# Kernel optimization log

Hardware: AMD Instinct MI355X
Metric: run time of the kernel (lower is better)

## Reference

```python
import jax, jax.numpy as jnp
import numpy as np

B, S, H = 8, 1024, 1024
NH, HD = 16, 64
LN_EPS = 1e-12


def setup_inputs() -> dict:
    key = jax.random.key(0)
    ks = jax.random.split(key, 8)
    sd = 0.02
    return {
        "hidden_states": jax.random.normal(ks[0], (B, S, H), jnp.float32),
        "attention_mask": jnp.zeros((B, 1, 1, S), jnp.float32),
        "Wq": jax.random.normal(ks[1], (H, H), jnp.float32) * sd,
        "bq": jnp.zeros((H,), jnp.float32),
        "Wk": jax.random.normal(ks[2], (H, H), jnp.float32) * sd,
        "bk": jnp.zeros((H,), jnp.float32),
        "Wv": jax.random.normal(ks[3], (H, H), jnp.float32) * sd,
        "bv": jnp.zeros((H,), jnp.float32),
        "Wo": jax.random.normal(ks[4], (H, H), jnp.float32) * sd,
        "bo": jnp.zeros((H,), jnp.float32),
        "ln_gamma": jnp.ones((H,), jnp.float32),
        "ln_beta": jnp.zeros((H,), jnp.float32),
    }


def _heads(x):
    # [B,S,H] -> [B,NH,S,HD]
    return x.reshape(B, S, NH, HD).transpose(0, 2, 1, 3)


def reference(hidden_states, attention_mask, Wq, bq, Wk, bk, Wv, bv, Wo, bo, ln_gamma, ln_beta):
    # QKV projections (torch Linear: x @ W.T + b)
    q = _heads(hidden_states @ Wq.T + bq)
    k = _heads(hidden_states @ Wk.T + bk)
    v = _heads(hidden_states @ Wv.T + bv)
    # scaled dot-product attention with additive mask
    scores = jnp.einsum("bhqd,bhkd->bhqk", q, k) / np.sqrt(HD).astype(np.float32)
    scores = scores + attention_mask  # broadcast [B,1,1,S]
    probs = jax.nn.softmax(scores, axis=-1)
    ctx = jnp.einsum("bhqk,bhkd->bhqd", probs, v)
    ctx = ctx.transpose(0, 2, 1, 3).reshape(B, S, H)
    # output projection + residual + LayerNorm
    out = ctx @ Wo.T + bo
    x = out + hidden_states
    mu = jnp.mean(x, axis=-1, keepdims=True)
    var = jnp.var(x, axis=-1, keepdims=True)
    return (x - mu) * jax.lax.rsqrt(var + LN_EPS) * ln_gamma + ln_beta
```

## Files before the change

### kernel.cpp

```cpp
#include <hip/hip_runtime.h>
#include <stdint.h>

typedef __attribute__((ext_vector_type(8))) __bf16 bf16x8;
typedef __attribute__((ext_vector_type(8))) unsigned short ushortx8;
typedef __attribute__((ext_vector_type(4))) unsigned short ushortx4;
typedef __attribute__((ext_vector_type(4))) short short4v;
typedef __attribute__((ext_vector_type(4))) float floatx4;

#define LOG2E 1.4426950408889634f
#define QSCALE 0.18033688011112043f

#define ASYNC16(g, l) __builtin_amdgcn_global_load_lds( \
    (__attribute__((address_space(1))) void*)(g),       \
    (__attribute__((address_space(3))) void*)(l), 16, 0, 0)

__device__ __forceinline__ unsigned short f2bf(float f) {
    unsigned int u = __float_as_uint(f);
    u += 0x7fffu + ((u >> 16) & 1u);
    return (unsigned short)(u >> 16);
}
__device__ __forceinline__ float bf2f(unsigned short u) {
    return __uint_as_float((unsigned)u << 16);
}

__device__ __forceinline__ floatx4 mfma32(bf16x8 a, bf16x8 b, floatx4 c) {
    return __builtin_amdgcn_mfma_f32_16x16x32_bf16(a, b, c, 0, 0, 0);
}
__device__ __forceinline__ floatx4 mfma16(short4v a, short4v b, floatx4 c) {
    return __builtin_amdgcn_mfma_f32_16x16x16bf16_1k(a, b, c, 0, 0, 0);
}

__global__ __launch_bounds__(256) void cvt_all(
    const float* __restrict__ hidden,
    const float* __restrict__ Wq, const float* __restrict__ Wk,
    const float* __restrict__ Wv, const float* __restrict__ Wo,
    unsigned short* __restrict__ hid_bf,
    unsigned short* __restrict__ oqkv, unsigned short* __restrict__ oo)
{
    const float* src;
    unsigned short* dst;
    int i;
    if (blockIdx.x < 4096) {
        src = hidden; dst = hid_bf;
        i = blockIdx.x * 256 + threadIdx.x;
    } else {
        int blk = (blockIdx.x - 4096) >> 9;
        src = (blk == 0) ? Wq : (blk == 1) ? Wk : (blk == 2) ? Wv : Wo;
        dst = (blk == 3) ? oo : oqkv + (size_t)blk * 1048576;
        i = ((blockIdx.x - 4096) & 511) * 256 + threadIdx.x;
    }
    const float4* p = (const float4*)src + (size_t)i * 2;
    float4 a = p[0], b = p[1];
    ushortx8 o;
    o[0] = f2bf(a.x); o[1] = f2bf(a.y); o[2] = f2bf(a.z); o[3] = f2bf(a.w);
    o[4] = f2bf(b.x); o[5] = f2bf(b.y); o[6] = f2bf(b.z); o[7] = f2bf(b.w);
    *((ushortx8*)dst + i) = o;
}

template<bool SWAP>
__device__ __forceinline__ void kloop_dbuf(
    const unsigned short* __restrict__ Ag,
    const unsigned short* __restrict__ Wg,
    unsigned short As[2][8192], unsigned short Bs[2][8192],
    int wm, int wn, int l16, int quad, int t,
    floatx4 acc[4][4])
{
    const int t8 = t * 8;
#define SAx(bf_, i_, kt_) ASYNC16(Ag + (size_t)(i_) * 32 * 1024 + (kt_) * 64, &As[bf_][(i_) * 2048 + t8])
#define SBx(bf_, i_, kt_) ASYNC16(Wg + (size_t)(i_) * 32 * 1024 + (kt_) * 64, &Bs[bf_][(i_) * 2048 + t8])
#pragma unroll
    for (int i = 0; i < 4; i++) { SAx(0, i, 0); SBx(0, i, 0); }
    __syncthreads();

#pragma unroll 1
    for (int kt = 0; kt < 16; ++kt) {
        const int cur = kt & 1, nb = cur ^ 1;
        if (kt < 15) {
#pragma unroll
            for (int i = 0; i < 4; i++) { SAx(nb, i, kt + 1); SBx(nb, i, kt + 1); }
        }
#pragma unroll
        for (int s = 0; s < 2; s++) {
            int pb = ((s * 4 + quad) ^ (l16 & 7)) * 8;
            bf16x8 af[4], bfr[4];
#pragma unroll
            for (int mt = 0; mt < 4; mt++)
                af[mt] = *(const bf16x8*)(&As[cur][(wm + mt * 16 + l16) * 64 + pb]);
#pragma unroll
            for (int nt = 0; nt < 4; nt++)
                bfr[nt] = *(const bf16x8*)(&Bs[cur][(wn + nt * 16 + l16) * 64 + pb]);
            if (SWAP) {
#pragma unroll
                for (int ft = 0; ft < 4; ft++)
#pragma unroll
                    for (int st = 0; st < 4; st++)
                        acc[ft][st] = mfma32(bfr[ft], af[st], acc[ft][st]);
            } else {
#pragma unroll
                for (int mt = 0; mt < 4; mt++)
#pragma unroll
                    for (int nt = 0; nt < 4; nt++)
                        acc[mt][nt] = mfma32(af[mt], bfr[nt], acc[mt][nt]);
            }
        }
        __syncthreads();
    }
#undef SAx
#undef SBx
}

__global__ __launch_bounds__(256, 2) void gemm_qkv(
    const unsigned short* __restrict__ A,
    const unsigned short* __restrict__ W,
    const float* __restrict__ bq, const float* __restrict__ bk, const float* __restrict__ bv,
    unsigned short* __restrict__ Qo, unsigned short* __restrict__ Ko,
    unsigned short* __restrict__ Vo)
{
    __shared__ unsigned short As[2][8192];
    __shared__ unsigned short Bs[2][8192];
    const int t = threadIdx.x;
    const int wave = t >> 6, lane = t & 63;
    const int quad = lane >> 4, l16 = lane & 15;
    const int wm = (wave >> 1) * 64, wn = (wave & 1) * 64;
    const int srow = t >> 3;
    const int scol = ((t & 7) ^ (srow & 7)) * 8;
    const int t8 = t * 8;

    const unsigned short* Ag = A + ((size_t)blockIdx.x * 128 + srow) * 1024 + scol;
    const unsigned short* Wg = W + ((size_t)blockIdx.y * 256 + srow) * 1024 + scol;

#define SA(bf_, i_, kt_) ASYNC16(Ag + (size_t)(i_) * 32768 + (kt_) * 64, &As[bf_][(i_) * 2048 + t8])
#define SB(rb_, i_, rp_, kt_) ASYNC16(Wg + (size_t)(rp_) * 131072 + (size_t)(i_) * 32768 + (kt_) * 64, \
                                      &Bs[rb_][(i_) * 2048 + t8])

#pragma unroll
    for (int i = 0; i < 4; i++) { SA(0, i, 0); SB(0, i, 0, 0); }
    __syncthreads();

    floatx4 acc[2][4][4] = {};

#pragma unroll 1
    for (int kt = 0; kt < 16; ++kt) {
        const int cur = kt & 1, nb = cur ^ 1;

#pragma unroll
        for (int i = 0; i < 4; i++) SB(1, i, 1, kt);
#pragma unroll
        for (int s = 0; s < 2; s++) {
            int pb = ((s * 4 + quad) ^ (l16 & 7)) * 8;
            bf16x8 af[4], bfr[4];
#pragma unroll
            for (int mt = 0; mt < 4; mt++)
                af[mt] = *(const bf16x8*)(&As[cur][(wm + mt * 16 + l16) * 64 + pb]);
#pragma unroll
            for (int ft = 0; ft < 4; ft++)
                bfr[ft] = *(const bf16x8*)(&Bs[0][(wn + ft * 16 + l16) * 64 + pb]);
#pragma unroll
            for (int ft = 0; ft < 4; ft++)
#pragma unroll
                for (int st = 0; st < 4; st++)
                    acc[0][ft][st] = mfma32(bfr[ft], af[st], acc[0][ft][st]);
        }
        __syncthreads();

        if (kt < 15) {
#pragma unroll
            for (int i = 0; i < 4; i++) { SB(0, i, 0, kt + 1); SA(nb, i, kt + 1); }
        }
#pragma unroll
        for (int s = 0; s < 2; s++) {
            int pb = ((s * 4 + quad) ^ (l16 & 7)) * 8;
            bf16x8 af[4], bfr[4];
#pragma unroll
            for (int mt = 0; mt < 4; mt++)
                af[mt] = *(const bf16x8*)(&As[cur][(wm + mt * 16 + l16) * 64 + pb]);
#pragma unroll
            for (int ft = 0; ft < 4; ft++)
                bfr[ft] = *(const bf16x8*)(&Bs[1][(wn + ft * 16 + l16) * 64 + pb]);
#pragma unroll
            for (int ft = 0; ft < 4; ft++)
#pragma unroll
                for (int st = 0; st < 4; st++)
                    acc[1][ft][st] = mfma32(bfr[ft], af[st], acc[1][ft][st]);
        }
        __syncthreads();
    }
#undef SA
#undef SB

#pragma unroll
    for (int rp = 0; rp < 2; ++rp) {
#pragma unroll
    for (int ft = 0; ft < 4; ++ft) {
        const int featg = blockIdx.y * 256 + rp * 128 + wn + ft * 16 + quad * 4;
        const int mat = featg >> 10;
        const int fin = featg & 1023;
        if (mat < 2) {
            const float* bp = (mat == 0) ? bq : bk;
            unsigned short* op = (mat == 0) ? Qo : Ko;
            const float sc = (mat == 0) ? QSCALE : 1.0f;
            const float4 b4 = *(const float4*)(bp + fin);
            const int h = fin >> 6, d = fin & 63;
#pragma unroll
            for (int st = 0; st < 4; ++st) {
                const int sg = blockIdx.x * 128 + wm + st * 16 + l16;
                const int b = sg >> 10, s = sg & 1023;
                ushortx4 o4;
                o4[0] = f2bf((acc[rp][ft][st][0] + b4.x) * sc);
                o4[1] = f2bf((acc[rp][ft][st][1] + b4.y) * sc);
                o4[2] = f2bf((acc[rp][ft][st][2] + b4.z) * sc);
                o4[3] = f2bf((acc[rp][ft][st][3] + b4.w) * sc);
                *(ushortx4*)(op + (((size_t)(b * 16 + h) * 1024 + s) * 64 + d)) = o4;
            }
        } else {
            const float4 b4 = *(const float4*)(bv + fin);
#pragma unroll
            for (int r = 0; r < 4; ++r) {
                const int fr = fin + r;
                const int h = fr >> 6, d = fr & 63;
                const float bias = (r == 0) ? b4.x : (r == 1) ? b4.y : (r == 2) ? b4.z : b4.w;
#pragma unroll
                for (int st = 0; st < 4; ++st) {
                    const int sg = blockIdx.x * 128 + wm + st * 16 + l16;
                    const int b = sg >> 10, s = sg & 1023;
                    const int sp = (s & ~63) + (st >> 1) * 32 + (l16 >> 2) * 8 +
                                   (st & 1) * 4 + (l16 & 3);
                    Vo[((size_t)(b * 16 + h) * 64 + d) * 1024 + sp] = f2bf(acc[rp][ft][st][r] + bias);
                }
            }
        }
    }
    }
}

__global__ __launch_bounds__(256) void attn(
    const unsigned short* __restrict__ Q,
    const unsigned short* __restrict__ Kg,
    const unsigned short* __restrict__ Vt,
    const float* __restrict__ mask,
    unsigned short* __restrict__ ctx)
{
    __shared__ unsigned short Ks[64 * 64];
    __shared__ unsigned short Vs[64 * 64];
    __shared__ float Msall[1024];

    const int t = threadIdx.x;
    const int wave = t >> 6, lane = t & 63, quad = lane >> 4, l16 = lane & 15;
    const int s7 = l16 & 7;
    const int head = blockIdx.x;
    const int b = head >> 4, h = head & 15;
    const int q0 = blockIdx.y * 128;
    const unsigned short* Qh = Q + (size_t)head * 65536;
    const unsigned short* Kh = Kg + (size_t)head * 65536;
    const unsigned short* Vh = Vt + (size_t)head * 65536;

    const int srow = t >> 3;
    const int scol = ((t & 7) ^ (srow & 7)) * 8;

    {
        float4 m4 = *(const float4*)(mask + b * 1024 + t * 4);
        m4.x *= LOG2E; m4.y *= LOG2E; m4.z *= LOG2E; m4.w *= LOG2E;
        *(float4*)(Msall + t * 4) = m4;
    }

    bf16x8 qf[2][2];
#pragma unroll
    for (int qg = 0; qg < 2; qg++) {
        const unsigned short* qp = Qh + (size_t)(q0 + wave * 32 + qg * 16 + l16) * 64 + quad * 8;
        qf[qg][0] = *(const bf16x8*)(qp);
        qf[qg][1] = *(const bf16x8*)(qp + 32);
    }

    const short4v ones = {(short)0x3F80, (short)0x3F80, (short)0x3F80, (short)0x3F80};
    floatx4 sum_acc[2] = {};
    floatx4 o_acc[2][4] = {};

    for (int k0 = 0; k0 < 1024; k0 += 64) {
        __syncthreads();
#pragma unroll
        for (int i = 0; i < 2; i++) {
            ASYNC16(Kh + (size_t)(k0 + i * 32 + srow) * 64 + scol, Ks + i * 2048 + t * 8);
            ASYNC16(Vh + (size_t)(i * 32 + srow) * 1024 + k0 + scol, Vs + i * 2048 + t * 8);
        }
        __syncthreads();

        short4v pf0[4], pf1[4];
#pragma unroll
        for (int nt = 0; nt < 4; nt++) {
            int krow = nt * 16 + l16;
            bf16x8 kf0 = *(const bf16x8*)(Ks + krow * 64 + ((quad ^ s7) * 8));
            bf16x8 kf1 = *(const bf16x8*)(Ks + krow * 64 + (((4 + quad) ^ s7) * 8));
            floatx4 mk = *(const floatx4*)(Msall + k0 + nt * 16 + quad * 4);
            floatx4 z0 = mk;
            z0 = mfma32(kf0, qf[0][0], z0);
            z0 = mfma32(kf1, qf[0][1], z0);
            floatx4 z1 = mk;
            z1 = mfma32(kf0, qf[1][0], z1);
            z1 = mfma32(kf1, qf[1][1], z1);
#pragma unroll
            for (int r = 0; r < 4; r++) {
                pf0[nt][r] = (short)(__float_as_uint(exp2f(z0[r])) >> 16);
                pf1[nt][r] = (short)(__float_as_uint(exp2f(z1[r])) >> 16);
            }
            sum_acc[0] = mfma16(ones, pf0[nt], sum_acc[0]);
            sum_acc[1] = mfma16(ones, pf1[nt], sum_acc[1]);
        }

#pragma unroll
        for (int dt = 0; dt < 4; dt++) {
            int vrow = dt * 16 + l16;
            ushortx8 v01 = *(const ushortx8*)(Vs + vrow * 64 + ((quad ^ s7) * 8));
            ushortx8 v23 = *(const ushortx8*)(Vs + vrow * 64 + (((4 + quad) ^ s7) * 8));
            short4v vf0 = {(short)v01[0], (short)v01[1], (short)v01[2], (short)v01[3]};
            short4v vf1 = {(short)v01[4], (short)v01[5], (short)v01[6], (short)v01[7]};
            short4v vf2 = {(short)v23[0], (short)v23[1], (short)v23[2], (short)v23[3]};
            short4v vf3 = {(short)v23[4], (short)v23[5], (short)v23[6], (short)v23[7]};
            o_acc[0][dt] = mfma16(vf0, pf0[0], o_acc[0][dt]);
            o_acc[0][dt] = mfma16(vf1, pf0[1], o_acc[0][dt]);
            o_acc[0][dt] = mfma16(vf2, pf0[2], o_acc[0][dt]);
            o_acc[0][dt] = mfma16(vf3, pf0[3], o_acc[0][dt]);
            o_acc[1][dt] = mfma16(vf0, pf1[0], o_acc[1][dt]);
            o_acc[1][dt] = mfma16(vf1, pf1[1], o_acc[1][dt]);
            o_acc[1][dt] = mfma16(vf2, pf1[2], o_acc[1][dt]);
            o_acc[1][dt] = mfma16(vf3, pf1[3], o_acc[1][dt]);
        }
    }

#pragma unroll
    for (int qg = 0; qg < 2; qg++) {
        float inv_l = 1.0f / sum_acc[qg][0];
        int qrow = q0 + wave * 32 + qg * 16 + l16;
#pragma unroll
        for (int dt = 0; dt < 4; dt++) {
            ushortx4 o4;
#pragma unroll
            for (int r = 0; r < 4; r++) o4[r] = f2bf(o_acc[qg][dt][r] * inv_l);
            *(ushortx4*)(ctx + ((size_t)(b * 1024 + qrow)) * 1024 + h * 64 + dt * 16 + quad * 4) = o4;
        }
    }
}

__global__ __launch_bounds__(256) void gemm_proj(
    const unsigned short* __restrict__ A,
    const unsigned short* __restrict__ W,
    const float* __restrict__ bo,
    const unsigned short* __restrict__ resid,
    unsigned short* __restrict__ X)
{
    __shared__ unsigned short As[2][8192];
    __shared__ unsigned short Bs[2][8192];
    const int t = threadIdx.x;
    const int wave = t >> 6, lane = t & 63;
    const int quad = lane >> 4, l16 = lane & 15;
    const int wm = (wave >> 1) * 64, wn = (wave & 1) * 64;
    const int srow = t >> 3;
    const int scol = ((t & 7) ^ (srow & 7)) * 8;

    const unsigned short* Ag = A + ((size_t)blockIdx.x * 128 + srow) * 1024 + scol;
    const unsigned short* Wg = W + ((size_t)blockIdx.y * 128 + srow) * 1024 + scol;

    floatx4 acc[4][4] = {};
    kloop_dbuf<false>(Ag, Wg, As, Bs, wm, wn, l16, quad, t, acc);

#pragma unroll
    for (int nt = 0; nt < 4; nt++) {
        int gn = blockIdx.y * 128 + wn + nt * 16 + l16;
        float bias = bo[gn];
#pragma unroll
        for (int mt = 0; mt < 4; mt++) {
#pragma unroll
            for (int r = 0; r < 4; r++) {
                int gm = blockIdx.x * 128 + wm + mt * 16 + quad * 4 + r;
                size_t off = (size_t)gm * 1024 + gn;
                X[off] = f2bf(acc[mt][nt][r] + bias + bf2f(resid[off]));
            }
        }
    }
}

__global__ __launch_bounds__(256) void ln_k(const unsigned short* __restrict__ X,
                                            const float* __restrict__ g,
                                            const float* __restrict__ be,
                                            float* __restrict__ out)
{
    int row = blockIdx.x;
    int t = threadIdx.x;
    const unsigned short* xr = X + (size_t)row * 1024;
    ushortx4 xb = *(const ushortx4*)(xr + t * 4);
    float4 v;
    v.x = bf2f(xb[0]);
    v.y = bf2f(xb[1]);
    v.z = bf2f(xb[2]);
    v.w = bf2f(xb[3]);
    float s = v.x + v.y + v.z + v.w;
    float ss = v.x * v.x + v.y * v.y + v.z * v.z + v.w * v.w;
    for (int off = 1; off < 64; off <<= 1) {
        s += __shfl_xor(s, off);
        ss += __shfl_xor(ss, off);
    }
    __shared__ float red[8];
    int wave = t >> 6, lane = t & 63;
    if (lane == 0) { red[wave] = s; red[4 + wave] = ss; }
    __syncthreads();
    s = red[0] + red[1] + red[2] + red[3];
    ss = red[4] + red[5] + red[6] + red[7];
    float mu = s * (1.f / 1024.f);
    float var = ss * (1.f / 1024.f) - mu * mu;
    float inv = rsqrtf(var + 1e-12f);
    float4 gv = *(const float4*)(g + t * 4);
    float4 bv = *(const float4*)(be + t * 4);
    float4 o;
    o.x = (v.x - mu) * inv * gv.x + bv.x;
    o.y = (v.y - mu) * inv * gv.y + bv.y;
    o.z = (v.z - mu) * inv * gv.z + bv.z;
    o.w = (v.w - mu) * inv * gv.w + bv.w;
    *(float4*)(out + (size_t)row * 1024 + t * 4) = o;
}

extern "C" void kernel_launch(void* const* d_in, const int* in_sizes, int n_in,
                              void* d_out, int out_size, void* d_ws, size_t ws_size,
                              hipStream_t stream)
{
    const float* hidden = (const float*)d_in[0];
    const float* mask   = (const float*)d_in[1];
    const float* Wq = (const float*)d_in[2];
    const float* bq = (const float*)d_in[3];
    const float* Wk = (const float*)d_in[4];
    const float* bk = (const float*)d_in[5];
    const float* Wv = (const float*)d_in[6];
    const float* bv = (const float*)d_in[7];
    const float* Wo = (const float*)d_in[8];
    const float* bo = (const float*)d_in[9];
    const float* gamma = (const float*)d_in[10];
    const float* beta  = (const float*)d_in[11];
    float* out = (float*)d_out;

    char* ws = (char*)d_ws;
    unsigned short* hid_bf  = (unsigned short*)(ws + 0);
    unsigned short* wqkv_bf = (unsigned short*)(ws + 16777216);
    unsigned short* wo_bf   = (unsigned short*)(ws + 23068672);
    unsigned short* vt_bf   = (unsigned short*)(ws + 25165824);
    unsigned short* ctx_bf  = (unsigned short*)(ws + 41943040);
    unsigned short* q_bf    = (unsigned short*)(ws + 58720256);
    unsigned short* k_bf    = (unsigned short*)(ws + 75497472);
    unsigned short* x_bf    = (unsigned short*)(ws + 58720256);

    cvt_all<<<6144, 256, 0, stream>>>(hidden, Wq, Wk, Wv, Wo, hid_bf, wqkv_bf, wo_bf);

    gemm_qkv<<<dim3(64, 12), 256, 0, stream>>>(hid_bf, wqkv_bf, bq, bk, bv, q_bf, k_bf, vt_bf);
    attn<<<dim3(128, 8), 256, 0, stream>>>(q_bf, k_bf, vt_bf, mask, ctx_bf);
    gemm_proj<<<dim3(64, 8), 256, 0, stream>>>(ctx_bf, wo_bf, bo, hid_bf, x_bf);
    ln_k<<<8192, 256, 0, stream>>>(x_bf, gamma, beta, out);
}
```

Before: 269.8 us.

## Widen QKV GEMM block tile to 128x384 with rotating B buffers

```diff
diff --git a/kernel.cpp b/kernel.cpp
--- a/kernel.cpp
+++ b/kernel.cpp
@@ -126,73 +126,68 @@
     const int scol = ((t & 7) ^ (srow & 7)) * 8;
     const int t8 = t * 8;
 
-    const unsigned short* Ag = A + ((size_t)blockIdx.x * 128 + srow) * 1024 + scol;
-    const unsigned short* Wg = W + ((size_t)blockIdx.y * 256 + srow) * 1024 + scol;
-
-#define SA(bf_, i_, kt_) ASYNC16(Ag + (size_t)(i_) * 32768 + (kt_) * 64, &As[bf_][(i_) * 2048 + t8])
-#define SB(rb_, i_, rp_, kt_) ASYNC16(Wg + (size_t)(rp_) * 131072 + (size_t)(i_) * 32768 + (kt_) * 64, \
+    const unsigned short* Ab = A + ((size_t)blockIdx.x * 128 + srow) * 1024 + scol;
+    const unsigned short* Wb = W + ((size_t)blockIdx.y * 384 + srow) * 1024 + scol;
+
+#define SA(bf_, i_, kt_) ASYNC16(Ab + (size_t)(i_) * 32768 + (kt_) * 64, &As[bf_][(i_) * 2048 + t8])
+#define SB(rb_, i_, rp_, kt_) ASYNC16(Wb + (size_t)(rp_) * 131072 + (size_t)(i_) * 32768 + (kt_) * 64, \
                                       &Bs[rb_][(i_) * 2048 + t8])
+#define REPC(RP, BB)                                                                   \
+    do {                                                                               \
+        _Pragma("unroll")                                                              \
+        for (int s = 0; s < 2; s++) {                                                  \
+            int pb = ((s * 4 + quad) ^ (l16 & 7)) * 8;                                 \
+            bf16x8 af[4], bfr[4];                                                      \
+            _Pragma("unroll")                                                          \
+            for (int mt = 0; mt < 4; mt++)                                             \
+                af[mt] = *(const bf16x8*)(&As[cur][(wm + mt * 16 + l16) * 64 + pb]);   \
+            _Pragma("unroll")                                                          \
+            for (int ft = 0; ft < 4; ft++)                                             \
+                bfr[ft] = *(const bf16x8*)(&Bs[BB][(wn + ft * 16 + l16) * 64 + pb]);   \
+            _Pragma("unroll")                                                          \
+            for (int ft = 0; ft < 4; ft++)                                             \
+                _Pragma("unroll")                                                      \
+                for (int st = 0; st < 4; st++)                                         \
+                    acc[RP][ft][st] = mfma32(bfr[ft], af[st], acc[RP][ft][st]);        \
+        }                                                                              \
+    } while (0)
 
 #pragma unroll
     for (int i = 0; i < 4; i++) { SA(0, i, 0); SB(0, i, 0, 0); }
     __syncthreads();
 
-    floatx4 acc[2][4][4] = {};
+    floatx4 acc[3][4][4] = {};
 
 #pragma unroll 1
     for (int kt = 0; kt < 16; ++kt) {
         const int cur = kt & 1, nb = cur ^ 1;
 
 #pragma unroll
-        for (int i = 0; i < 4; i++) SB(1, i, 1, kt);
-#pragma unroll
-        for (int s = 0; s < 2; s++) {
-            int pb = ((s * 4 + quad) ^ (l16 & 7)) * 8;
-            bf16x8 af[4], bfr[4];
-#pragma unroll
-            for (int mt = 0; mt < 4; mt++)
-                af[mt] = *(const bf16x8*)(&As[cur][(wm + mt * 16 + l16) * 64 + pb]);
-#pragma unroll
-            for (int ft = 0; ft < 4; ft++)
-                bfr[ft] = *(const bf16x8*)(&Bs[0][(wn + ft * 16 + l16) * 64 + pb]);
-#pragma unroll
-            for (int ft = 0; ft < 4; ft++)
-#pragma unroll
-                for (int st = 0; st < 4; st++)
-                    acc[0][ft][st] = mfma32(bfr[ft], af[st], acc[0][ft][st]);
-        }
+        for (int i = 0; i < 4; i++) SB(nb, i, 1, kt);
+        REPC(0, cur);
+        __syncthreads();
+
+#pragma unroll
+        for (int i = 0; i < 4; i++) SB(cur, i, 2, kt);
+        REPC(1, nb);
         __syncthreads();
 
         if (kt < 15) {
 #pragma unroll
-            for (int i = 0; i < 4; i++) { SB(0, i, 0, kt + 1); SA(nb, i, kt + 1); }
-        }
-#pragma unroll
-        for (int s = 0; s < 2; s++) {
-            int pb = ((s * 4 + quad) ^ (l16 & 7)) * 8;
-            bf16x8 af[4], bfr[4];
-#pragma unroll
-            for (int mt = 0; mt < 4; mt++)
-                af[mt] = *(const bf16x8*)(&As[cur][(wm + mt * 16 + l16) * 64 + pb]);
-#pragma unroll
-            for (int ft = 0; ft < 4; ft++)
-                bfr[ft] = *(const bf16x8*)(&Bs[1][(wn + ft * 16 + l16) * 64 + pb]);
-#pragma unroll
-            for (int ft = 0; ft < 4; ft++)
-#pragma unroll
-                for (int st = 0; st < 4; st++)
-                    acc[1][ft][st] = mfma32(bfr[ft], af[st], acc[1][ft][st]);
-        }
-        __syncthreads();
-    }
+            for (int i = 0; i < 4; i++) { SB(nb, i, 0, kt + 1); SA(nb, i, kt + 1); }
+        }
+        REPC(2, cur);
+        __syncthreads();
+    }
+#undef REPC
 #undef SA
 #undef SB
 
 #pragma unroll
-    for (int rp = 0; rp < 2; ++rp) {
+    for (int rp = 0; rp < 3; ++rp) {
 #pragma unroll
     for (int ft = 0; ft < 4; ++ft) {
-        const int featg = blockIdx.y * 256 + rp * 128 + wn + ft * 16 + quad * 4;
+        const int featg = blockIdx.y * 384 + rp * 128 + wn + ft * 16 + quad * 4;
         const int mat = featg >> 10;
         const int fin = featg & 1023;
         if (mat < 2) {
@@ -447,7 +442,7 @@
 
     cvt_all<<<6144, 256, 0, stream>>>(hidden, Wq, Wk, Wv, Wo, hid_bf, wqkv_bf, wo_bf);
 
-    gemm_qkv<<<dim3(64, 12), 256, 0, stream>>>(hid_bf, wqkv_bf, bq, bk, bv, q_bf, k_bf, vt_bf);
+    gemm_qkv<<<dim3(64, 8), 256, 0, stream>>>(hid_bf, wqkv_bf, bq, bk, bv, q_bf, k_bf, vt_bf);
     attn<<<dim3(128, 8), 256, 0, stream>>>(q_bf, k_bf, vt_bf, mask, ctx_bf);
     gemm_proj<<<dim3(64, 8), 256, 0, stream>>>(ctx_bf, wo_bf, bo, hid_bf, x_bf);
     ln_k<<<8192, 256, 0, stream>>>(x_bf, gamma, beta, out);
```

Measured after the change: 259.5 us. -3.8%, faster.
